# Optimization experiments

Measured on AMD Instinct MI355X. Metric: run time of the kernel, lower is better.

Reference implementation:

```python
import jax, jax.numpy as jnp
import numpy as np

B, S, VD, MD = 32, 2048, 512, 512
AD = max(VD, MD)


def setup_inputs() -> dict:
    key = jax.random.key(0)
    k1, k2, k3, k4, k5, k6 = jax.random.split(key, 6)
    query = jax.random.normal(k1, (B, VD), dtype=jnp.float32)
    keys = jax.random.normal(k2, (B, S, MD), dtype=jnp.float32)
    mask = jax.random.randint(k3, (B, S), 0, 2).astype(jnp.bool_)
    # torch Linear weight layout: [out, in]
    W1 = jax.random.normal(k4, (AD, VD), dtype=jnp.float32) * (1.0 / np.sqrt(VD))
    W2 = jax.random.normal(k5, (AD, MD), dtype=jnp.float32) * (1.0 / np.sqrt(MD))
    v = jax.random.normal(k6, (AD,), dtype=jnp.float32) * (1.0 / np.sqrt(AD))
    return {"query": query, "keys": keys, "mask": mask, "W1": W1, "W2": W2, "v": v}


def reference(query, keys, mask, W1, W2, v):
    # w1_query: [B, 1, AD]; w2_keys: [B, S, AD]
    w1_query = jnp.einsum('bd,ad->ba', query, W1)[:, None, :]
    w2_keys = jnp.einsum('bsd,ad->bsa', keys, W2)
    combined = jnp.tanh(w1_query + w2_keys)            # [B, S, AD]
    scores = jnp.einsum('bsa,a->bs', combined, v)      # [B, S]
    scores = jnp.where(mask, scores, -jnp.inf)
    attn_weights = jax.nn.softmax(scores, axis=-1)
    return attn_weights
```

## Files before the change

kernel.cpp:

```cpp
#include <hip/hip_runtime.h>
#include <math.h>

#define BB 32
#define SS 2048
#define DD 512
#define AD 512

#define BM 128
#define BN 128
#define BK 64

typedef __bf16 bf16;
typedef __attribute__((ext_vector_type(8))) __bf16 bf16x8;
typedef __attribute__((ext_vector_type(4))) __bf16 bf16x4;
typedef __attribute__((ext_vector_type(4))) float floatx4;

__device__ inline void async16(const void* g, void* l) {
    __builtin_amdgcn_global_load_lds(
        (const __attribute__((address_space(1))) unsigned int*)g,
        (__attribute__((address_space(3))) unsigned int*)l, 16, 0, 0);
}

#define NW8 (AD * DD / 8)
#define NCV (NW8 / 256)
__global__ void prep_kernel(const float* __restrict__ W2,
                            bf16* __restrict__ W2b,
                            const unsigned char* __restrict__ m8,
                            int* __restrict__ flag,
                            const float* __restrict__ query,
                            const float* __restrict__ W1,
                            float* __restrict__ w1q) {
    const int bid = blockIdx.x;
    if (bid < NCV) {
        int j = threadIdx.x + bid * 256;
        const float4* s4 = (const float4*)W2 + (size_t)j * 2;
        float4 x = s4[0], y = s4[1];
        bf16x8 o;
        o[0] = (bf16)x.x; o[1] = (bf16)x.y; o[2] = (bf16)x.z; o[3] = (bf16)x.w;
        o[4] = (bf16)y.x; o[5] = (bf16)y.y; o[6] = (bf16)y.z; o[7] = (bf16)y.w;
        *(bf16x8*)(W2b + (size_t)j * 8) = o;
    } else if (bid < NCV + 64) {
        int t = threadIdx.x + (bid - NCV) * 256;
        int any = 0;
        for (int i = t; i < BB * SS; i += 64 * 256)
            if ((i & 3) && m8[i]) any = 1;
        if (__any(any)) {
            if ((threadIdx.x & 63) == 0) atomicOr(flag, 1);
        }
    } else {
        int id = bid - NCV - 64;
        int b = id >> 7;
        int a = (id & 127) * 4 + (threadIdx.x >> 6);
        int lane = threadIdx.x & 63;
        const float4* q4 = (const float4*)(query + (size_t)b * DD) + lane * 2;
        const float4* w4 = (const float4*)(W1 + (size_t)a * DD) + lane * 2;
        float4 qa = q4[0], qb = q4[1];
        float4 wa = w4[0], wb = w4[1];
        float acc = qa.x * wa.x + qa.y * wa.y + qa.z * wa.z + qa.w * wa.w
                  + qb.x * wb.x + qb.y * wb.y + qb.z * wb.z + qb.w * wb.w;
#pragma unroll
        for (int off = 32; off > 0; off >>= 1) acc += __shfl_down(acc, off);
        if (lane == 0) w1q[(size_t)b * AD + a] = acc;
    }
}

__global__ __launch_bounds__(256, 2)
void gemm_scores_mfma(const float* __restrict__ keys,
                      const bf16* __restrict__ W2b,
                      const float* __restrict__ w1q,
                      const float* __restrict__ v,
                      float* __restrict__ partial) {
    __shared__ bf16 a_lds[2][BM * BK];
    __shared__ bf16 b_lds[2][BN * BK];

    const int t    = threadIdx.x;
    const int lane = t & 63;
    const int w    = t >> 6;
    const int ml   = lane & 15;
    const int kg   = lane >> 4;

    const int lin    = blockIdx.x;
    const int x8     = lin & 7;
    const int hi     = lin >> 3;
    const int a_tile = hi & 3;
    const int kt     = x8 + ((hi >> 2) << 3);
    const int b      = kt >> 4;
    const int s0     = (kt & 15) * BM;
    const int a0     = a_tile * BN;

    const int m_off = (w & 1) * 64;
    const int n_off = (w >> 1) * 64;

    const float* Ablk = keys + ((size_t)b * SS + s0) * DD;
    const bf16*  Bblk = W2b + (size_t)a0 * DD;

    floatx4 acc[4][4];
#pragma unroll
    for (int mi = 0; mi < 4; ++mi)
#pragma unroll
        for (int ni = 0; ni < 4; ++ni)
            acc[mi][ni] = (floatx4)(0.f);

    int ar[4], ac8[4], acs[4];
#pragma unroll
    for (int j = 0; j < 4; ++j) {
        int u = t + 256 * j;
        ar[j]  = u >> 3;
        ac8[j] = (u & 7) * 8;
        acs[j] = ((u & 7) ^ (ar[j] & 7)) * 8;
    }

    const int NCHUNK = DD / BK;
    float4 areg[4][2];

#pragma unroll
    for (int j = 0; j < 4; ++j) {
        const float* src = Ablk + (size_t)ar[j] * DD + ac8[j];
        areg[j][0] = *(const float4*)src;
        areg[j][1] = *(const float4*)(src + 4);
    }
#pragma unroll
    for (int i = 0; i < 4; ++i) {
        int g = t + 256 * i;
        int r = g >> 3, cc = g & 7, cs = cc ^ (r & 7);
        async16(Bblk + (size_t)r * DD + cs * 8,
                &b_lds[0][(256 * i + 64 * w) * 8]);
    }
#pragma unroll
    for (int j = 0; j < 4; ++j) {
        bf16x8 o;
        o[0] = (bf16)areg[j][0].x; o[1] = (bf16)areg[j][0].y;
        o[2] = (bf16)areg[j][0].z; o[3] = (bf16)areg[j][0].w;
        o[4] = (bf16)areg[j][1].x; o[5] = (bf16)areg[j][1].y;
        o[6] = (bf16)areg[j][1].z; o[7] = (bf16)areg[j][1].w;
        *(bf16x8*)&a_lds[0][ar[j] * BK + acs[j]] = o;
    }

    for (int c = 0; c < NCHUNK; ++c) {
        const int cur = c & 1;
        const int nxt = cur ^ 1;
        __syncthreads();

        if (c + 1 < NCHUNK) {
            const int d0 = (c + 1) * BK;
#pragma unroll
            for (int j = 0; j < 4; ++j) {
                const float* src = Ablk + (size_t)ar[j] * DD + d0 + ac8[j];
                areg[j][0] = *(const float4*)src;
                areg[j][1] = *(const float4*)(src + 4);
            }
#pragma unroll
            for (int i = 0; i < 4; ++i) {
                int g = t + 256 * i;
                int r = g >> 3, cc = g & 7, cs = cc ^ (r & 7);
                async16(Bblk + (size_t)r * DD + d0 + cs * 8,
                        &b_lds[nxt][(256 * i + 64 * w) * 8]);
            }
        }

#pragma unroll
        for (int ks = 0; ks < 2; ++ks) {
            bf16x8 af[4], bfr[4];
#pragma unroll
            for (int mi = 0; mi < 4; ++mi) {
                int R = m_off + mi * 16 + ml;
                int p = (ks * 4 + kg) ^ (R & 7);
                af[mi] = *(const bf16x8*)&a_lds[cur][R * BK + p * 8];
            }
#pragma unroll
            for (int ni = 0; ni < 4; ++ni) {
                int R = n_off + ni * 16 + ml;
                int p = (ks * 4 + kg) ^ (R & 7);
                bfr[ni] = *(const bf16x8*)&b_lds[cur][R * BK + p * 8];
            }
#pragma unroll
            for (int mi = 0; mi < 4; ++mi)
#pragma unroll
                for (int ni = 0; ni < 4; ++ni)
                    acc[mi][ni] = __builtin_amdgcn_mfma_f32_16x16x32_bf16(
                        af[mi], bfr[ni], acc[mi][ni], 0, 0, 0);
        }

        __builtin_amdgcn_sched_barrier(0);
        if (c + 1 < NCHUNK) {
#pragma unroll
            for (int j = 0; j < 4; ++j) {
                bf16x8 o;
                o[0] = (bf16)areg[j][0].x; o[1] = (bf16)areg[j][0].y;
                o[2] = (bf16)areg[j][0].z; o[3] = (bf16)areg[j][0].w;
                o[4] = (bf16)areg[j][1].x; o[5] = (bf16)areg[j][1].y;
                o[6] = (bf16)areg[j][1].z; o[7] = (bf16)areg[j][1].w;
                *(bf16x8*)&a_lds[nxt][ar[j] * BK + acs[j]] = o;
            }
        }
    }

    float w1qa[4], va[4];
#pragma unroll
    for (int ni = 0; ni < 4; ++ni) {
        int a = a0 + n_off + ni * 16 + ml;
        w1qa[ni] = w1q[(size_t)b * AD + a];
        va[ni]   = v[a];
    }
    const int slot = a_tile * 2 + (w >> 1);
#pragma unroll
    for (int mi = 0; mi < 4; ++mi) {
#pragma unroll
        for (int reg = 0; reg < 4; ++reg) {
            float p = 0.f;
#pragma unroll
            for (int ni = 0; ni < 4; ++ni) {
                float x = acc[mi][ni][reg] + w1qa[ni];
                float th = 1.f - 2.f / (1.f + __expf(2.f * x));
                p = fmaf(th, va[ni], p);
            }
            p += __shfl_xor(p, 1);
            p += __shfl_xor(p, 2);
            p += __shfl_xor(p, 4);
            p += __shfl_xor(p, 8);
            if (ml == 0) {
                int row = m_off + mi * 16 + kg * 4 + reg;
                partial[((size_t)b * SS + s0 + row) * 8 + slot] = p;
            }
        }
    }
}

#define FBK 32
#define FLDK (FBK + 8)
__global__ __launch_bounds__(256, 2)
void gemm_scores_fallback(const float* __restrict__ keys,
                          const float* __restrict__ W2,
                          const float* __restrict__ w1q,
                          const float* __restrict__ v,
                          float* __restrict__ partial) {
    __shared__ bf16 a_lds[BM][FLDK];
    __shared__ bf16 b_lds[BN][FLDK];
    __shared__ float s_red[BM];

    const int t    = threadIdx.x;
    const int lane = t & 63;
    const int w    = t >> 6;
    const int ml   = lane & 15;
    const int kg   = lane >> 4;
    const int b    = blockIdx.z;
    const int s0   = blockIdx.x * BM;
    const int a0   = blockIdx.y * BN;
    const int m_off = (w & 1) * 64;
    const int n_off = (w >> 1) * 64;

    const float* Ablk = keys + ((size_t)b * SS + s0) * DD;
    const float* Bblk = W2 + (size_t)a0 * DD;

    if (t < BM) s_red[t] = 0.f;

    floatx4 acc[4][4];
#pragma unroll
    for (int mi = 0; mi < 4; ++mi)
#pragma unroll
        for (int ni = 0; ni < 4; ++ni)
            acc[mi][ni] = (floatx4)(0.f);

    float4 ga[4], gb[4];
#pragma unroll
    for (int i = 0; i < 4; ++i) {
        int idx = t + 256 * i;
        int r = idx >> 3, c = idx & 7;
        ga[i] = *(const float4*)(Ablk + (size_t)r * DD + c * 4);
        gb[i] = *(const float4*)(Bblk + (size_t)r * DD + c * 4);
    }

    for (int chunk = 0; chunk < DD / FBK; ++chunk) {
        __syncthreads();
#pragma unroll
        for (int i = 0; i < 4; ++i) {
            int idx = t + 256 * i;
            int r = idx >> 3, c = idx & 7;
            bf16x4 pa, pb;
            pa[0] = (bf16)ga[i].x; pa[1] = (bf16)ga[i].y;
            pa[2] = (bf16)ga[i].z; pa[3] = (bf16)ga[i].w;
            pb[0] = (bf16)gb[i].x; pb[1] = (bf16)gb[i].y;
            pb[2] = (bf16)gb[i].z; pb[3] = (bf16)gb[i].w;
            *(bf16x4*)&a_lds[r][c * 4] = pa;
            *(bf16x4*)&b_lds[r][c * 4] = pb;
        }
        __syncthreads();
        if (chunk < DD / FBK - 1) {
            int d0 = (chunk + 1) * FBK;
#pragma unroll
            for (int i = 0; i < 4; ++i) {
                int idx = t + 256 * i;
                int r = idx >> 3, c = idx & 7;
                ga[i] = *(const float4*)(Ablk + (size_t)r * DD + d0 + c * 4);
                gb[i] = *(const float4*)(Bblk + (size_t)r * DD + d0 + c * 4);
            }
        }
        bf16x8 af[4], bfr[4];
#pragma unroll
        for (int mi = 0; mi < 4; ++mi)
            af[mi] = *(const bf16x8*)&a_lds[m_off + mi * 16 + ml][kg * 8];
#pragma unroll
        for (int ni = 0; ni < 4; ++ni)
            bfr[ni] = *(const bf16x8*)&b_lds[n_off + ni * 16 + ml][kg * 8];
#pragma unroll
        for (int mi = 0; mi < 4; ++mi)
#pragma unroll
            for (int ni = 0; ni < 4; ++ni)
                acc[mi][ni] = __builtin_amdgcn_mfma_f32_16x16x32_bf16(
                    af[mi], bfr[ni], acc[mi][ni], 0, 0, 0);
    }

    float w1qa[4], va[4];
#pragma unroll
    for (int ni = 0; ni < 4; ++ni) {
        int a = a0 + n_off + ni * 16 + ml;
        w1qa[ni] = w1q[(size_t)b * AD + a];
        va[ni]   = v[a];
    }
#pragma unroll
    for (int mi = 0; mi < 4; ++mi) {
#pragma unroll
        for (int reg = 0; reg < 4; ++reg) {
            float p = 0.f;
#pragma unroll
            for (int ni = 0; ni < 4; ++ni) {
                float x = acc[mi][ni][reg] + w1qa[ni];
                float th = 1.f - 2.f / (1.f + __expf(2.f * x));
                p = fmaf(th, va[ni], p);
            }
            p += __shfl_xor(p, 1);
            p += __shfl_xor(p, 2);
            p += __shfl_xor(p, 4);
            p += __shfl_xor(p, 8);
            if (ml == 0)
                atomicAdd(&s_red[m_off + mi * 16 + kg * 4 + reg], p);
        }
    }
    __syncthreads();
    if (t < BM)
        partial[(((size_t)b * SS) + s0 + t) * 8 + blockIdx.y * 2] = s_red[t];
}

__global__ void softmax_kernel(const float* __restrict__ partial,
                               const int* __restrict__ mask_i32,
                               const unsigned char* __restrict__ mask_u8,
                               const int* __restrict__ flag,
                               float* __restrict__ out) {
    const int b = blockIdx.x;
    const int t = threadIdx.x;
    __shared__ float rmax[4], rsum[4];
    const int wid = t >> 6, lane = t & 63;

    float sv[8]; int mv[8];
    const int bytes = (*flag != 0);
#pragma unroll
    for (int k = 0; k < 8; ++k) {
        int i = t + 256 * k;
        const float4* p4 = (const float4*)(partial + ((size_t)b * SS + i) * 8);
        float4 pa = p4[0], pb = p4[1];
        sv[k] = ((pa.x + pa.y) + (pa.z + pa.w)) + ((pb.x + pb.y) + (pb.z + pb.w));
        mv[k] = bytes ? (int)mask_u8[(size_t)b * SS + i]
                      : mask_i32[(size_t)b * SS + i];
    }

    float mx = -INFINITY;
#pragma unroll
    for (int k = 0; k < 8; ++k) mx = fmaxf(mx, mv[k] ? sv[k] : -INFINITY);
#pragma unroll
    for (int off = 32; off > 0; off >>= 1) mx = fmaxf(mx, __shfl_xor(mx, off));
    if (lane == 0) rmax[wid] = mx;
    __syncthreads();
    mx = fmaxf(fmaxf(rmax[0], rmax[1]), fmaxf(rmax[2], rmax[3]));

    float ev[8]; float sum = 0.f;
#pragma unroll
    for (int k = 0; k < 8; ++k) {
        ev[k] = mv[k] ? __expf(sv[k] - mx) : 0.f;
        sum += ev[k];
    }
#pragma unroll
    for (int off = 32; off > 0; off >>= 1) sum += __shfl_xor(sum, off);
    if (lane == 0) rsum[wid] = sum;
    __syncthreads();
    sum = (rsum[0] + rsum[1]) + (rsum[2] + rsum[3]);
    float inv = 1.f / sum;
#pragma unroll
    for (int k = 0; k < 8; ++k)
        out[(size_t)b * SS + t + 256 * k] = ev[k] * inv;
}

extern "C" void kernel_launch(void* const* d_in, const int* in_sizes, int n_in,
                              void* d_out, int out_size, void* d_ws, size_t ws_size,
                              hipStream_t stream) {
    const float* query = (const float*)d_in[0];
    const float* keys  = (const float*)d_in[1];
    const void*  mask  = d_in[2];
    const float* W1    = (const float*)d_in[3];
    const float* W2    = (const float*)d_in[4];
    const float* v     = (const float*)d_in[5];
    float* out = (float*)d_out;

    char* wsb = (char*)d_ws;
    int*   flag    = (int*)wsb;
    float* w1q     = (float*)(wsb + 256);
    float* partial = (float*)(wsb + 256 + 65536);
    bf16*  W2b     = (bf16*)(wsb + 256 + 65536 + 2097152);
    size_t need = 256 + 65536 + 2097152 + (size_t)AD * DD * 2;

    hipMemsetAsync(flag, 0, 4, stream);
    if (ws_size >= need) {
        prep_kernel<<<NCV + 64 + 4096, 256, 0, stream>>>(
            W2, W2b, (const unsigned char*)mask, flag, query, W1, w1q);
        gemm_scores_mfma<<<(SS / BM) * (AD / BN) * BB, 256, 0, stream>>>(
            keys, W2b, w1q, v, partial);
    } else {
        hipMemsetAsync(partial, 0, (size_t)BB * SS * 8 * 4, stream);
        prep_kernel<<<NCV + 64 + 4096, 256, 0, stream>>>(
            W2, W2b, (const unsigned char*)mask, flag, query, W1, w1q);
        gemm_scores_fallback<<<dim3(SS / BM, AD / BN, BB), 256, 0, stream>>>(
            keys, W2, w1q, v, partial);
    }
    softmax_kernel<<<BB, 256, 0, stream>>>(partial, (const int*)mask,
                                           (const unsigned char*)mask, flag, out);
}
```

Measured before the change: 261.1 us.

## Fuse query projection into MFMA GEMM and move mask detection into softmax

```diff
diff --git a/kernel.cpp b/kernel.cpp
--- a/kernel.cpp
+++ b/kernel.cpp
@@ -22,55 +22,45 @@
 }
 
 #define NW8 (AD * DD / 8)
-#define NCV (NW8 / 256)
-__global__ void prep_kernel(const float* __restrict__ W2,
-                            bf16* __restrict__ W2b,
-                            const unsigned char* __restrict__ m8,
-                            int* __restrict__ flag,
-                            const float* __restrict__ query,
-                            const float* __restrict__ W1,
-                            float* __restrict__ w1q) {
-    const int bid = blockIdx.x;
-    if (bid < NCV) {
-        int j = threadIdx.x + bid * 256;
-        const float4* s4 = (const float4*)W2 + (size_t)j * 2;
-        float4 x = s4[0], y = s4[1];
-        bf16x8 o;
-        o[0] = (bf16)x.x; o[1] = (bf16)x.y; o[2] = (bf16)x.z; o[3] = (bf16)x.w;
-        o[4] = (bf16)y.x; o[5] = (bf16)y.y; o[6] = (bf16)y.z; o[7] = (bf16)y.w;
-        *(bf16x8*)(W2b + (size_t)j * 8) = o;
-    } else if (bid < NCV + 64) {
-        int t = threadIdx.x + (bid - NCV) * 256;
-        int any = 0;
-        for (int i = t; i < BB * SS; i += 64 * 256)
-            if ((i & 3) && m8[i]) any = 1;
-        if (__any(any)) {
-            if ((threadIdx.x & 63) == 0) atomicOr(flag, 1);
-        }
-    } else {
-        int id = bid - NCV - 64;
-        int b = id >> 7;
-        int a = (id & 127) * 4 + (threadIdx.x >> 6);
-        int lane = threadIdx.x & 63;
-        const float4* q4 = (const float4*)(query + (size_t)b * DD) + lane * 2;
-        const float4* w4 = (const float4*)(W1 + (size_t)a * DD) + lane * 2;
-        float4 qa = q4[0], qb = q4[1];
-        float4 wa = w4[0], wb = w4[1];
-        float acc = qa.x * wa.x + qa.y * wa.y + qa.z * wa.z + qa.w * wa.w
-                  + qb.x * wb.x + qb.y * wb.y + qb.z * wb.z + qb.w * wb.w;
-#pragma unroll
-        for (int off = 32; off > 0; off >>= 1) acc += __shfl_down(acc, off);
-        if (lane == 0) w1q[(size_t)b * AD + a] = acc;
-    }
-}
-
-__global__ __launch_bounds__(256, 2)
+__global__ void convert_kernel(const float* __restrict__ W2,
+                               const float* __restrict__ W1,
+                               bf16* __restrict__ Wb) {
+    int j = threadIdx.x + blockIdx.x * 256;
+    const float* src = (j < NW8) ? (W2 + (size_t)j * 8)
+                                 : (W1 + (size_t)(j - NW8) * 8);
+    const float4* s4 = (const float4*)src;
+    float4 x = s4[0], y = s4[1];
+    bf16x8 o;
+    o[0] = (bf16)x.x; o[1] = (bf16)x.y; o[2] = (bf16)x.z; o[3] = (bf16)x.w;
+    o[4] = (bf16)y.x; o[5] = (bf16)y.y; o[6] = (bf16)y.z; o[7] = (bf16)y.w;
+    *(bf16x8*)(Wb + (size_t)j * 8) = o;
+}
+
+__global__ void w1q_kernel(const float* __restrict__ query,
+                           const float* __restrict__ W1,
+                           float* __restrict__ w1q) {
+    int id = blockIdx.x;
+    int b = id >> 7;
+    int a = (id & 127) * 4 + (threadIdx.x >> 6);
+    int lane = threadIdx.x & 63;
+    const float4* q4 = (const float4*)(query + (size_t)b * DD) + lane * 2;
+    const float4* w4 = (const float4*)(W1 + (size_t)a * DD) + lane * 2;
+    float4 qa = q4[0], qb = q4[1];
+    float4 wa = w4[0], wb = w4[1];
+    float acc = qa.x * wa.x + qa.y * wa.y + qa.z * wa.z + qa.w * wa.w
+              + qb.x * wb.x + qb.y * wb.y + qb.z * wb.z + qb.w * wb.w;
+#pragma unroll
+    for (int off = 32; off > 0; off >>= 1) acc += __shfl_down(acc, off);
+    if (lane == 0) w1q[(size_t)b * AD + a] = acc;
+}
+
+__global__ __launch_bounds__(256, 3)
 void gemm_scores_mfma(const float* __restrict__ keys,
-                      const bf16* __restrict__ W2b,
-                      const float* __restrict__ w1q,
+                      const bf16* __restrict__ Wb,
+                      const float* __restrict__ query,
                       const float* __restrict__ v,
                       float* __restrict__ partial) {
-    __shared__ bf16 a_lds[2][BM * BK];
+    __shared__ bf16 a_lds[BM * BK];
     __shared__ bf16 b_lds[2][BN * BK];
 
     const int t    = threadIdx.x;
@@ -92,14 +82,18 @@
     const int n_off = (w >> 1) * 64;
 
     const float* Ablk = keys + ((size_t)b * SS + s0) * DD;
-    const bf16*  Bblk = W2b + (size_t)a0 * DD;
+    const bf16*  Bblk = Wb + (size_t)a0 * DD;
+    const float* qrow = query + (size_t)b * DD;
 
     floatx4 acc[4][4];
+    floatx4 accW[4];
 #pragma unroll
     for (int mi = 0; mi < 4; ++mi)
 #pragma unroll
         for (int ni = 0; ni < 4; ++ni)
             acc[mi][ni] = (floatx4)(0.f);
+#pragma unroll
+    for (int ni = 0; ni < 4; ++ni) accW[ni] = (floatx4)(0.f);
 
     int ar[4], ac8[4], acs[4];
 #pragma unroll
@@ -110,7 +104,6 @@
         acs[j] = ((u & 7) ^ (ar[j] & 7)) * 8;
     }
 
-    const int NCHUNK = DD / BK;
     float4 areg[4][2];
 
 #pragma unroll
@@ -122,9 +115,16 @@
 #pragma unroll
     for (int i = 0; i < 4; ++i) {
         int g = t + 256 * i;
-        int r = g >> 3, cc = g & 7, cs = cc ^ (r & 7);
+        int r = g >> 3, cs = (g & 7) ^ (r & 7);
         async16(Bblk + (size_t)r * DD + cs * 8,
                 &b_lds[0][(256 * i + 64 * w) * 8]);
+    }
+#pragma unroll
+    for (int i = 0; i < 4; ++i) {
+        int g = t + 256 * i;
+        int r = g >> 3, cs = (g & 7) ^ (r & 7);
+        async16(Bblk + (size_t)r * DD + BK + cs * 8,
+                &b_lds[1][(256 * i + 64 * w) * 8]);
     }
 #pragma unroll
     for (int j = 0; j < 4; ++j) {
@@ -133,56 +133,90 @@
         o[2] = (bf16)areg[j][0].z; o[3] = (bf16)areg[j][0].w;
         o[4] = (bf16)areg[j][1].x; o[5] = (bf16)areg[j][1].y;
         o[6] = (bf16)areg[j][1].z; o[7] = (bf16)areg[j][1].w;
-        *(bf16x8*)&a_lds[0][ar[j] * BK + acs[j]] = o;
-    }
-
-    for (int c = 0; c < NCHUNK; ++c) {
-        const int cur = c & 1;
-        const int nxt = cur ^ 1;
-        __syncthreads();
-
-        if (c + 1 < NCHUNK) {
-            const int d0 = (c + 1) * BK;
+        *(bf16x8*)&a_lds[ar[j] * BK + acs[j]] = o;
+    }
+    __syncthreads();
+
+    for (int c = 0; c < 16; ++c) {
+        const int ca = c + 1;
+        if (ca < 8) {
+            const int d0a = ca * BK;
 #pragma unroll
             for (int j = 0; j < 4; ++j) {
-                const float* src = Ablk + (size_t)ar[j] * DD + d0 + ac8[j];
+                const float* src = Ablk + (size_t)ar[j] * DD + d0a + ac8[j];
                 areg[j][0] = *(const float4*)src;
                 areg[j][1] = *(const float4*)(src + 4);
             }
+        }
+
+        if (c < 8) {
+#pragma unroll
+            for (int ks = 0; ks < 2; ++ks) {
+                bf16x8 af[4], bfr[4];
+#pragma unroll
+                for (int mi = 0; mi < 4; ++mi) {
+                    int R = m_off + mi * 16 + ml;
+                    int p = (ks * 4 + kg) ^ (R & 7);
+                    af[mi] = *(const bf16x8*)&a_lds[R * BK + p * 8];
+                }
+#pragma unroll
+                for (int ni = 0; ni < 4; ++ni) {
+                    int R = n_off + ni * 16 + ml;
+                    int p = (ks * 4 + kg) ^ (R & 7);
+                    bfr[ni] = *(const bf16x8*)&b_lds[c & 1][R * BK + p * 8];
+                }
+#pragma unroll
+                for (int mi = 0; mi < 4; ++mi)
+#pragma unroll
+                    for (int ni = 0; ni < 4; ++ni)
+                        acc[mi][ni] = __builtin_amdgcn_mfma_f32_16x16x32_bf16(
+                            af[mi], bfr[ni], acc[mi][ni], 0, 0, 0);
+            }
+        } else {
+            const int dq = (c - 8) * BK;
+            float4 q0a = *(const float4*)(qrow + dq + kg * 8);
+            float4 q0b = *(const float4*)(qrow + dq + kg * 8 + 4);
+            float4 q1a = *(const float4*)(qrow + dq + 32 + kg * 8);
+            float4 q1b = *(const float4*)(qrow + dq + 32 + kg * 8 + 4);
+#pragma unroll
+            for (int ks = 0; ks < 2; ++ks) {
+                float4 qa = ks ? q1a : q0a;
+                float4 qb = ks ? q1b : q0b;
+                bf16x8 af;
+                af[0] = (bf16)qa.x; af[1] = (bf16)qa.y;
+                af[2] = (bf16)qa.z; af[3] = (bf16)qa.w;
+                af[4] = (bf16)qb.x; af[5] = (bf16)qb.y;
+                af[6] = (bf16)qb.z; af[7] = (bf16)qb.w;
+                bf16x8 bfr[4];
+#pragma unroll
+                for (int ni = 0; ni < 4; ++ni) {
+                    int R = n_off + ni * 16 + ml;
+                    int p = (ks * 4 + kg) ^ (R & 7);
+                    bfr[ni] = *(const bf16x8*)&b_lds[c & 1][R * BK + p * 8];
+                }
+#pragma unroll
+                for (int ni = 0; ni < 4; ++ni)
+                    accW[ni] = __builtin_amdgcn_mfma_f32_16x16x32_bf16(
+                        af, bfr[ni], accW[ni], 0, 0, 0);
+            }
+        }
+
+        __builtin_amdgcn_sched_barrier(0);
+        __syncthreads();
+
+        if (c + 2 <= 15) {
+            const int cn2  = c + 2;
+            const size_t koff = (cn2 >= 8) ? (size_t)AD * DD : 0;
+            const int d0b = (cn2 & 7) * BK;
 #pragma unroll
             for (int i = 0; i < 4; ++i) {
                 int g = t + 256 * i;
-                int r = g >> 3, cc = g & 7, cs = cc ^ (r & 7);
-                async16(Bblk + (size_t)r * DD + d0 + cs * 8,
-                        &b_lds[nxt][(256 * i + 64 * w) * 8]);
-            }
-        }
-
-#pragma unroll
-        for (int ks = 0; ks < 2; ++ks) {
-            bf16x8 af[4], bfr[4];
-#pragma unroll
-            for (int mi = 0; mi < 4; ++mi) {
-                int R = m_off + mi * 16 + ml;
-                int p = (ks * 4 + kg) ^ (R & 7);
-                af[mi] = *(const bf16x8*)&a_lds[cur][R * BK + p * 8];
-            }
-#pragma unroll
-            for (int ni = 0; ni < 4; ++ni) {
-                int R = n_off + ni * 16 + ml;
-                int p = (ks * 4 + kg) ^ (R & 7);
-                bfr[ni] = *(const bf16x8*)&b_lds[cur][R * BK + p * 8];
-            }
-#pragma unroll
-            for (int mi = 0; mi < 4; ++mi)
-#pragma unroll
-                for (int ni = 0; ni < 4; ++ni)
-                    acc[mi][ni] = __builtin_amdgcn_mfma_f32_16x16x32_bf16(
-                        af[mi], bfr[ni], acc[mi][ni], 0, 0, 0);
-        }
-
-        __builtin_amdgcn_sched_barrier(0);
-        if (c + 1 < NCHUNK) {
+                int r = g >> 3, cs = (g & 7) ^ (r & 7);
+                async16(Bblk + koff + (size_t)r * DD + d0b + cs * 8,
+                        &b_lds[c & 1][(256 * i + 64 * w) * 8]);
+            }
+        }
+        if (ca < 8) {
 #pragma unroll
             for (int j = 0; j < 4; ++j) {
                 bf16x8 o;
@@ -190,18 +224,15 @@
                 o[2] = (bf16)areg[j][0].z; o[3] = (bf16)areg[j][0].w;
                 o[4] = (bf16)areg[j][1].x; o[5] = (bf16)areg[j][1].y;
                 o[6] = (bf16)areg[j][1].z; o[7] = (bf16)areg[j][1].w;
-                *(bf16x8*)&a_lds[nxt][ar[j] * BK + acs[j]] = o;
-            }
-        }
-    }
-
-    float w1qa[4], va[4];
-#pragma unroll
-    for (int ni = 0; ni < 4; ++ni) {
-        int a = a0 + n_off + ni * 16 + ml;
-        w1qa[ni] = w1q[(size_t)b * AD + a];
-        va[ni]   = v[a];
-    }
+                *(bf16x8*)&a_lds[ar[j] * BK + acs[j]] = o;
+            }
+        }
+        __syncthreads();
+    }
+
+    float va[4];
+#pragma unroll
+    for (int ni = 0; ni < 4; ++ni) va[ni] = v[a0 + n_off + ni * 16 + ml];
     const int slot = a_tile * 2 + (w >> 1);
 #pragma unroll
     for (int mi = 0; mi < 4; ++mi) {
@@ -210,7 +241,7 @@
             float p = 0.f;
 #pragma unroll
             for (int ni = 0; ni < 4; ++ni) {
-                float x = acc[mi][ni][reg] + w1qa[ni];
+                float x = acc[mi][ni][reg] + accW[ni][0];
                 float th = 1.f - 2.f / (1.f + __expf(2.f * x));
                 p = fmaf(th, va[ni], p);
             }
@@ -342,25 +373,40 @@
 }
 
 __global__ void softmax_kernel(const float* __restrict__ partial,
-                               const int* __restrict__ mask_i32,
-                               const unsigned char* __restrict__ mask_u8,
-                               const int* __restrict__ flag,
+                               const void* __restrict__ mask,
                                float* __restrict__ out) {
     const int b = blockIdx.x;
     const int t = threadIdx.x;
     __shared__ float rmax[4], rsum[4];
+    __shared__ int s_bytes;
     const int wid = t >> 6, lane = t & 63;
 
+    if (t == 0) s_bytes = 0;
+    __syncthreads();
+    {
+        const uint4* m16 = (const uint4*)mask;
+        unsigned pr = 0;
+#pragma unroll
+        for (int k = 0; k < 16; ++k) {
+            uint4 x = m16[t + 256 * k];
+            pr |= (x.x | x.y | x.z | x.w) & 0xFFFFFF00u;
+        }
+        if (pr) s_bytes = 1;
+    }
+    __syncthreads();
+    const int bytes = s_bytes;
+    const unsigned char* m8  = (const unsigned char*)mask;
+    const int*           m32 = (const int*)mask;
+
     float sv[8]; int mv[8];
-    const int bytes = (*flag != 0);
 #pragma unroll
     for (int k = 0; k < 8; ++k) {
         int i = t + 256 * k;
         const float4* p4 = (const float4*)(partial + ((size_t)b * SS + i) * 8);
         float4 pa = p4[0], pb = p4[1];
         sv[k] = ((pa.x + pa.y) + (pa.z + pa.w)) + ((pb.x + pb.y) + (pb.z + pb.w));
-        mv[k] = bytes ? (int)mask_u8[(size_t)b * SS + i]
-                      : mask_i32[(size_t)b * SS + i];
+        mv[k] = bytes ? (int)m8[(size_t)b * SS + i]
+                      : m32[(size_t)b * SS + i];
     }
 
     float mx = -INFINITY;
@@ -401,25 +447,22 @@
     float* out = (float*)d_out;
 
     char* wsb = (char*)d_ws;
-    int*   flag    = (int*)wsb;
-    float* w1q     = (float*)(wsb + 256);
-    float* partial = (float*)(wsb + 256 + 65536);
-    bf16*  W2b     = (bf16*)(wsb + 256 + 65536 + 2097152);
-    size_t need = 256 + 65536 + 2097152 + (size_t)AD * DD * 2;
-
-    hipMemsetAsync(flag, 0, 4, stream);
-    if (ws_size >= need) {
-        prep_kernel<<<NCV + 64 + 4096, 256, 0, stream>>>(
-            W2, W2b, (const unsigned char*)mask, flag, query, W1, w1q);
+    float* partial = (float*)(wsb + 256);
+    bf16*  Wb      = (bf16*)(wsb + 256 + 2097152);
+    size_t need_main = 256 + 2097152 + (size_t)2 * AD * DD * 2;
+
+    if (ws_size >= need_main) {
+        convert_kernel<<<256, 256, 0, stream>>>(W2, W1, Wb);
         gemm_scores_mfma<<<(SS / BM) * (AD / BN) * BB, 256, 0, stream>>>(
-            keys, W2b, w1q, v, partial);
+            keys, Wb, query, v, partial);
+        softmax_kernel<<<BB, 256, 0, stream>>>(partial, mask, out);
     } else {
-        hipMemsetAsync(partial, 0, (size_t)BB * SS * 8 * 4, stream);
-        prep_kernel<<<NCV + 64 + 4096, 256, 0, stream>>>(
-            W2, W2b, (const unsigned char*)mask, flag, query, W1, w1q);
+        float* w1q        = (float*)(wsb + 256);
+        float* partial_fb = (float*)(wsb + 256 + 65536);
+        hipMemsetAsync(partial_fb, 0, (size_t)BB * SS * 8 * 4, stream);
+        w1q_kernel<<<4096, 256, 0, stream>>>(query, W1, w1q);
         gemm_scores_fallback<<<dim3(SS / BM, AD / BN, BB), 256, 0, stream>>>(
-            keys, W2, w1q, v, partial);
-    }
-    softmax_kernel<<<BB, 256, 0, stream>>>(partial, (const int*)mask,
-                                           (const unsigned char*)mask, flag, out);
-}
+            keys, W2, w1q, v, partial_fb);
+        softmax_kernel<<<BB, 256, 0, stream>>>(partial_fb, mask, out);
+    }
+}
```

Measured after the change: 347.4 us. +33.1%, slower.
